# Optimization experiments

Measured on AMD Instinct MI355X. Metric: run time of the kernel, lower is better.

## Reference

```python
import jax, jax.numpy as jnp
import numpy as np

# dims: batch, seq (<=300 due to tril buffer), raw embed, model dim (hardcoded 300), experts, heads, head_size
B, T, D_IN, D, E, H, HS = 64, 300, 768, 300, 8, 4, 16
TOP_K = E // 2


def setup_inputs() -> dict:
    key = jax.random.key(0)
    ks = jax.random.split(key, 10)
    f = lambda k, s, sc: jax.random.normal(k, s, jnp.float32) * sc
    return {
        "x": jax.random.normal(ks[0], (B, T, D_IN), jnp.float32),
        "wh_bias": jnp.zeros((D_IN,), jnp.float32),
        "wh_W": f(ks[1], (D, D_IN), 0.02),              # WhitenLayer linear (no bias)
        "Wq": f(ks[2], (H, HS, D), 0.05),                # stacked per-head query weights
        "Wk": f(ks[3], (H, HS, D), 0.05),
        "Wv": f(ks[4], (H, HS, D), 0.05),
        "proj_W": f(ks[5], (D, H * HS), 0.05),
        "proj_b": jnp.zeros((D,), jnp.float32),
        "exp_W1": f(ks[6], (E, 2 * D, D), (2.0 / (2 * D)) ** 0.5),  # kaiming fan_out
        "exp_b1": jnp.zeros((E, 2 * D), jnp.float32),
        "exp_W2": f(ks[7], (E, D, 2 * D), (2.0 / D) ** 0.5),
        "exp_b2": jnp.zeros((E, D), jnp.float32),
        "w_gate": f(ks[8], (D, E), 0.02),
    }


def reference(x, wh_bias, wh_W, Wq, Wk, Wv, proj_W, proj_b,
              exp_W1, exp_b1, exp_W2, exp_b2, w_gate):
    # WhitenLayer: lin(x - bias)  (dropout identity in eval)
    xw = jnp.einsum('btd,od->bto', x - wh_bias, wh_W)          # [B,T,D]

    # MultiHeadAttention (causal, scale = C**-0.5 with C = D = 300)
    q = jnp.einsum('btd,hkd->bhtk', xw, Wq)
    k = jnp.einsum('btd,hkd->bhtk', xw, Wk)
    v = jnp.einsum('btd,hkd->bhtk', xw, Wv)
    wei = jnp.einsum('bhtk,bhsk->bhts', q, k) * (D ** -0.5)
    tril = jnp.tril(jnp.ones((T, T), bool))
    wei = jax.nn.softmax(jnp.where(tril, wei, -jnp.inf), axis=-1)
    att = jnp.einsum('bhts,bhsk->bthk', wei, v).reshape(x.shape[0], T, H * HS)
    xa = att @ proj_W.T + proj_b                               # [B,T,D]

    # noisy_top_k_gating in eval mode (no noise); masked dispatch == dense weighted sum
    logits = xa @ w_gate                                       # [B,T,E]
    topv, topi = jax.lax.top_k(logits, TOP_K)
    sel = jax.nn.one_hot(topi, E, dtype=bool).any(axis=-2)     # [B,T,E] top-k mask
    sparse = jnp.where(sel, logits, -jnp.inf)
    gprob = jax.nn.softmax(sparse, axis=-1)                    # zero on non-selected

    # all experts applied densely (forward also recomputes them all anyway)
    h = jax.nn.relu(jnp.einsum('btd,ehd->bteh', xa, exp_W1) + exp_b1)
    eo = jnp.einsum('bteh,eoh->bteo', h, exp_W2) + exp_b2      # [B,T,E,D]

    gates = jnp.einsum('bte,bteo->bto', gprob, eo)             # dispatched mixture [B,T,D]
    # forward: (gates.unsqueeze(-2) * expert_outputs).sum(-2) == gates * sum_e expert_e
    return gates * eo.sum(axis=-2)
```

## Files before the change

kernel.cpp:

```cpp
#include <hip/hip_runtime.h>
#include <cstdint>
#include <cstddef>

#define B_   64
#define T_   300
#define DIN_ 768
#define D_   300
#define E_   8
#define NTOK (B_*T_)
#define TW   6
#define SC   32

typedef __attribute__((ext_vector_type(8))) short bf8_t;
typedef __attribute__((ext_vector_type(4))) float f4_t;

__device__ __forceinline__ unsigned short f2bf(float v) {
  union { float f; unsigned u; } a; a.f = v;
  unsigned r = a.u + 0x7fff + ((a.u >> 16) & 1);
  return (unsigned short)(r >> 16);
}
__device__ __forceinline__ float bf2f(unsigned short s) {
  union { float f; unsigned u; } a; a.u = ((unsigned)s) << 16; return a.f;
}
__device__ __forceinline__ void split3(float v, unsigned short& p0,
                                       unsigned short& p1, unsigned short& p2) {
  p0 = f2bf(v);
  float r1 = v - bf2f(p0);
  p1 = f2bf(r1);
  float r2 = r1 - bf2f(p1);
  p2 = f2bf(r2);
}
__device__ __forceinline__ void split2(float v, unsigned short& p0,
                                       unsigned short& p1) {
  p0 = f2bf(v);
  p1 = f2bf(v - bf2f(p0));
}

__device__ __forceinline__ void gld16(const unsigned short* g, unsigned short* l) {
  __builtin_amdgcn_global_load_lds(
      (const __attribute__((address_space(1))) unsigned int*)g,
      (__attribute__((address_space(3))) unsigned int*)l, 16, 0, 0);
}

__global__ void biasproj_kernel(const float* __restrict__ wh_bias,
                                const float* __restrict__ wh_W,
                                float* __restrict__ bp) {
  int o = blockIdx.x * blockDim.x + threadIdx.x;
  if (o >= D_) return;
  float acc = 0.f;
  const float* row = wh_W + (size_t)o * DIN_;
  for (int d = 0; d < DIN_; ++d) acc += wh_bias[d] * row[d];
  bp[o] = -acc;
}

__global__ void split_pad(const float* __restrict__ src, unsigned short* __restrict__ dst,
                          int rows, int K, int Kp, size_t planeStride, int np) {
  int n = rows * Kp;
  for (int i = blockIdx.x * blockDim.x + threadIdx.x; i < n; i += gridDim.x * blockDim.x) {
    int r = i / Kp, c = i % Kp;
    unsigned short p0 = 0, p1 = 0, p2 = 0;
    if (c < K) split3(src[(size_t)r * K + c], p0, p1, p2);
    dst[i] = p0;
    dst[planeStride + i] = p1;
    if (np == 3) dst[2 * planeStride + i] = p2;
  }
}

template<int AFP, int EPI, int JN, int WM, int NP, int NPO, int SWZ>
__global__ __launch_bounds__(WM * 64) void mfma_gen(
    const void* __restrict__ Av, size_t aPStride, int ldA,
    const unsigned short* __restrict__ Bg, size_t bPStride,
    const float* __restrict__ bias, float* __restrict__ C,
    unsigned short* __restrict__ Po, size_t poStride, int ldPo,
    float* __restrict__ gsum, float* __restrict__ esum,
    const float* __restrict__ gate,
    int M, int N, int K) {
  constexpr int TILE_M = WM * 32;
  constexpr int BROWS  = JN * 32;
  constexpr int APB    = TILE_M * 64;
  constexpr int BPB    = BROWS * 64;
  constexpr int AINSTS = NP * APB / 1024;
  constexpr int BINSTS = NP * BPB / 1024;
  static_assert(!AFP || NP == 3, "AFP path writes 3 planes");
  __shared__ unsigned short Ap[NP][TILE_M * 32];
  __shared__ unsigned short Bp[NP][BROWS * 32];
  const int tid = threadIdx.x;
  int bxv = blockIdx.x, byv = blockIdx.y;
  if constexpr (SWZ) {
    const int nx  = gridDim.x;
    const int nwg = nx * gridDim.y;
    const int id  = byv * nx + bxv;
    const int xcd = id & 7, idx = id >> 3;
    const int q = nwg >> 3, r = nwg & 7;
    const int nid = (xcd < r) ? (xcd * (q + 1) + idx)
                              : (r * (q + 1) + (xcd - r) * q + idx);
    bxv = nid % nx;
    byv = nid / nx;
  }
  const int bm = byv * TILE_M, bn = bxv * BROWS;
  const int widx = tid >> 6;
  const int wr = (widx >> 1) * 64;
  const int wc = (widx & 1) * (JN * 16);
  const int lane = tid & 63;
  const int lr = lane & 15;
  const int kg = lane >> 4;
  const int sw = (lr >> 1) & 3;
  const int Kp = (K + 31) & ~31;
  const int arow = tid >> 1, ahalf = (tid & 1) * 16;
  const int asw = (arow >> 1) & 3;

  auto stageB = [&](int k0) {
    for (int q = widx; q < BINSTS; q += WM) {
      const int f   = q * 1024 + lane * 16;
      const int pp  = f / BPB;
      const int rem = f % BPB;
      const int row = rem >> 6;
      const int cl  = ((rem >> 4) & 3) ^ ((row >> 1) & 3);
      int brow = bn + row; if (brow >= N) brow = N - 1;
      gld16(Bg + (size_t)pp * bPStride + (size_t)brow * Kp + k0 + cl * 8,
            (unsigned short*)Bp + q * 512);
    }
  };
  auto stageA = [&](int k0) {
    if constexpr (AFP) {
      const float* Arow = (const float*)Av + (size_t)(bm + arow) * ldA + k0 + ahalf;
      #pragma unroll
      for (int u = 0; u < 4; ++u) {
        float4 qv = *(const float4*)&Arow[u * 4];
        float vv[4] = {qv.x, qv.y, qv.z, qv.w};
        unsigned short s0[4], s1[4], s2[4];
        #pragma unroll
        for (int w = 0; w < 4; ++w) split3(vv[w], s0[w], s1[w], s2[w]);
        const int k  = ahalf + u * 4;
        const int so = arow * 32 + (((k >> 3) ^ asw) << 3) + (k & 7);
        *(unsigned*)&Ap[0][so]     = (unsigned)s0[0] | ((unsigned)s0[1] << 16);
        *(unsigned*)&Ap[0][so + 2] = (unsigned)s0[2] | ((unsigned)s0[3] << 16);
        *(unsigned*)&Ap[1][so]     = (unsigned)s1[0] | ((unsigned)s1[1] << 16);
        *(unsigned*)&Ap[1][so + 2] = (unsigned)s1[2] | ((unsigned)s1[3] << 16);
        *(unsigned*)&Ap[2][so]     = (unsigned)s2[0] | ((unsigned)s2[1] << 16);
        *(unsigned*)&Ap[2][so + 2] = (unsigned)s2[2] | ((unsigned)s2[3] << 16);
      }
    } else {
      for (int q = widx; q < AINSTS; q += WM) {
        const int f   = q * 1024 + lane * 16;
        const int pp  = f / APB;
        const int rem = f % APB;
        const int row = rem >> 6;
        const int cl  = ((rem >> 4) & 3) ^ ((row >> 1) & 3);
        gld16((const unsigned short*)Av + (size_t)pp * aPStride +
                  (size_t)(bm + row) * Kp + k0 + cl * 8,
              (unsigned short*)Ap + q * 512);
      }
    }
  };

  f4_t acc[4][JN];
  #pragma unroll
  for (int i = 0; i < 4; ++i)
    #pragma unroll
    for (int j = 0; j < JN; ++j) acc[i][j] = (f4_t){0.f, 0.f, 0.f, 0.f};

  stageB(0); stageA(0);
  __syncthreads();
  for (int k0 = 0; k0 < Kp; k0 += 32) {
    bf8_t a[4][NP], b[JN][NP];
    #pragma unroll
    for (int i = 0; i < 4; ++i)
      #pragma unroll
      for (int p = 0; p < NP; ++p)
        a[i][p] = *(const bf8_t*)&Ap[p][(wr + i * 16 + lr) * 32 + ((kg ^ sw) << 3)];
    #pragma unroll
    for (int j = 0; j < JN; ++j)
      #pragma unroll
      for (int p = 0; p < NP; ++p)
        b[j][p] = *(const bf8_t*)&Bp[p][(wc + j * 16 + lr) * 32 + ((kg ^ sw) << 3)];
    __syncthreads();
    if (k0 + 32 < Kp) { stageB(k0 + 32); stageA(k0 + 32); }
    #pragma unroll
    for (int i = 0; i < 4; ++i)
      #pragma unroll
      for (int j = 0; j < JN; ++j) {
        f4_t c = acc[i][j];
        if constexpr (NP == 3) {
          c = __builtin_amdgcn_mfma_f32_16x16x32_bf16(a[i][2], b[j][0], c, 0, 0, 0);
          c = __builtin_amdgcn_mfma_f32_16x16x32_bf16(a[i][1], b[j][1], c, 0, 0, 0);
          c = __builtin_amdgcn_mfma_f32_16x16x32_bf16(a[i][0], b[j][2], c, 0, 0, 0);
          c = __builtin_amdgcn_mfma_f32_16x16x32_bf16(a[i][1], b[j][0], c, 0, 0, 0);
          c = __builtin_amdgcn_mfma_f32_16x16x32_bf16(a[i][0], b[j][1], c, 0, 0, 0);
          c = __builtin_amdgcn_mfma_f32_16x16x32_bf16(a[i][0], b[j][0], c, 0, 0, 0);
        } else {
          c = __builtin_amdgcn_mfma_f32_16x16x32_bf16(a[i][1], b[j][0], c, 0, 0, 0);
          c = __builtin_amdgcn_mfma_f32_16x16x32_bf16(a[i][0], b[j][1], c, 0, 0, 0);
          c = __builtin_amdgcn_mfma_f32_16x16x32_bf16(a[i][0], b[j][0], c, 0, 0, 0);
        }
        acc[i][j] = c;
      }
    __syncthreads();
  }
  #pragma unroll
  for (int i = 0; i < 4; ++i) {
    #pragma unroll
    for (int r = 0; r < 4; ++r) {
      const int row = bm + wr + i * 16 + kg * 4 + r;
      float g = 0.f;
      if constexpr (EPI >= 2 && EPI <= 4) g = gate[(size_t)row * E_];
      #pragma unroll
      for (int j = 0; j < JN; ++j) {
        const int col = bn + wc + j * 16 + lr;
        float v = acc[i][j][r];
        if constexpr (EPI == 0) {
          if (col < N) {
            if (bias) v += bias[col];
            C[(size_t)row * N + col] = v;
          }
        } else if constexpr (EPI == 1 || EPI == 5 || EPI == 6) {
          if (col < ldPo) {
            unsigned short p0 = 0, p1 = 0, p2 = 0;
            if (col < N) {
              v += bias[col];
              if constexpr (EPI == 1) v = fmaxf(v, 0.f);
              if constexpr (EPI == 6) C[(size_t)row * N + col] = v;
              if constexpr (NPO == 3) split3(v, p0, p1, p2);
              else                    split2(v, p0, p1);
            }
            size_t o = (size_t)row * ldPo + col;
            Po[o] = p0;
            Po[poStride + o] = p1;
            if constexpr (NPO == 3) Po[2 * poStride + o] = p2;
          }
        } else {
          if (col < N) {
            float eo = v + bias[col];
            size_t idx = (size_t)row * N + col;
            if constexpr (EPI == 2) {
              gsum[idx] = g * eo;
              esum[idx] = eo;
            } else if constexpr (EPI == 3) {
              gsum[idx] += g * eo;
              esum[idx] += eo;
            } else {
              float gs = gsum[idx] + g * eo;
              float es = esum[idx] + eo;
              C[idx] = gs * es;
            }
          }
        }
      }
    }
  }
}

__global__ __launch_bounds__(64 * TW) void attn_kernel(
    const float* __restrict__ qkv, float* __restrict__ attout) {
  const int nch_blk = T_ / TW;
  const int b   = blockIdx.x / nch_blk;
  const int tch = blockIdx.x % nch_blk;
  const int w    = threadIdx.x >> 6;
  const int lane = threadIdx.x & 63;
  const int h = lane >> 4, li = lane & 15;
  const int t    = tch * TW + w;
  const int tmax = tch * TW + TW - 1;
  __shared__ float kv[SC][68];
  __shared__ float p[TW][4][304];
  const float scale = rsqrtf((float)D_);
  const float* base = qkv + (size_t)b * T_ * 192;
  const float* qrow = base + (size_t)t * 192 + h * 16;
  const float4 q0 = *(const float4*)(qrow);
  const float4 q1 = *(const float4*)(qrow + 4);
  const float4 q2 = *(const float4*)(qrow + 8);
  const float4 q3 = *(const float4*)(qrow + 12);
  const int nch = tmax / SC + 1;

  float mmax = -1e30f;
  for (int c = 0; c < nch; ++c) {
    const int s0 = c * SC;
    __syncthreads();
    for (int i = threadIdx.x; i < SC * 16; i += 64 * TW) {
      const int r = i >> 4, c4 = (i & 15) * 4;
      int sr = s0 + r; if (sr > T_ - 1) sr = T_ - 1;
      *(float4*)&kv[r][c4] = *(const float4*)&base[(size_t)sr * 192 + 64 + c4];
    }
    __syncthreads();
    const int send = (s0 + SC - 1 < t) ? s0 + SC - 1 : t;
    for (int s = s0 + li; s <= send; s += 16) {
      const float* kr = &kv[s - s0][h * 16];
      float4 k0 = *(const float4*)(kr);
      float4 k1 = *(const float4*)(kr + 4);
      float4 k2 = *(const float4*)(kr + 8);
      float4 k3 = *(const float4*)(kr + 12);
      float acc = q0.x * k0.x + q0.y * k0.y + q0.z * k0.z + q0.w * k0.w;
      acc += q1.x * k1.x + q1.y * k1.y + q1.z * k1.z + q1.w * k1.w;
      acc += q2.x * k2.x + q2.y * k2.y + q2.z * k2.z + q2.w * k2.w;
      acc += q3.x * k3.x + q3.y * k3.y + q3.z * k3.z + q3.w * k3.w;
      acc *= scale;
      p[w][h][s] = acc;
      mmax = fmaxf(mmax, acc);
    }
  }
  #pragma unroll
  for (int m = 8; m >= 1; m >>= 1) mmax = fmaxf(mmax, __shfl_xor(mmax, m, 16));
  float lsum = 0.f;
  for (int s = li; s <= t; s += 16) {
    float e = __expf(p[w][h][s] - mmax);
    p[w][h][s] = e;
    lsum += e;
  }
  #pragma unroll
  for (int m = 8; m >= 1; m >>= 1) lsum += __shfl_xor(lsum, m, 16);
  const float inv = 1.0f / lsum;

  float o0 = 0.f, o1 = 0.f, o2 = 0.f, o3 = 0.f;
  for (int c = 0; c < nch; ++c) {
    const int s0 = c * SC;
    __syncthreads();
    for (int i = threadIdx.x; i < SC * 16; i += 64 * TW) {
      const int r = i >> 4, c4 = (i & 15) * 4;
      int sr = s0 + r; if (sr > T_ - 1) sr = T_ - 1;
      *(float4*)&kv[r][c4] = *(const float4*)&base[(size_t)sr * 192 + 128 + c4];
    }
    __syncthreads();
    const int send = (s0 + SC - 1 < t) ? s0 + SC - 1 : t;
    const int col = h * 16 + li;
    int s = s0;
    for (; s + 3 <= send; s += 4) {
      float4 pw = *(const float4*)&p[w][h][s];
      o0 += pw.x * kv[s - s0][col];
      o1 += pw.y * kv[s + 1 - s0][col];
      o2 += pw.z * kv[s + 2 - s0][col];
      o3 += pw.w * kv[s + 3 - s0][col];
    }
    for (; s <= send; ++s) o0 += p[w][h][s] * kv[s - s0][col];
  }
  attout[((size_t)b * T_ + t) * 192 + lane] = ((o0 + o1) + (o2 + o3)) * inv;
}

__global__ void logits_kernel(const float* __restrict__ xa,
                              const float* __restrict__ w_gate,
                              float* __restrict__ logits) {
  int idx = blockIdx.x * blockDim.x + threadIdx.x;
  if (idx >= NTOK * E_) return;
  int n = idx >> 3, e = idx & 7;
  const float* xr = xa + (size_t)n * D_;
  float acc = 0.f;
  for (int d = 0; d < D_; ++d) acc += xr[d] * w_gate[(size_t)d * E_ + e];
  logits[idx] = acc;
}

__global__ void gate_kernel(const float* __restrict__ logits,
                            float* __restrict__ gprob) {
  int n = blockIdx.x * blockDim.x + threadIdx.x;
  if (n >= NTOK) return;
  float l[E_];
  #pragma unroll
  for (int e = 0; e < E_; ++e) l[e] = logits[(size_t)n * E_ + e];
  bool sel[E_] = {false, false, false, false, false, false, false, false};
  for (int kk = 0; kk < E_ / 2; ++kk) {
    int bi = -1; float bv = -1e38f;
    #pragma unroll
    for (int e = 0; e < E_; ++e)
      if (!sel[e] && l[e] > bv) { bv = l[e]; bi = e; }
    sel[bi] = true;
  }
  float mx = -1e38f;
  #pragma unroll
  for (int e = 0; e < E_; ++e) if (sel[e]) mx = fmaxf(mx, l[e]);
  float s = 0.f, pp[E_];
  #pragma unroll
  for (int e = 0; e < E_; ++e) {
    pp[e] = sel[e] ? __expf(l[e] - mx) : 0.f;
    s += pp[e];
  }
  float inv = 1.0f / s;
  #pragma unroll
  for (int e = 0; e < E_; ++e) gprob[(size_t)n * E_ + e] = pp[e] * inv;
}

extern "C" void kernel_launch(void* const* d_in, const int* in_sizes, int n_in,
                              void* d_out, int out_size, void* d_ws, size_t ws_size,
                              hipStream_t stream) {
  const float* x       = (const float*)d_in[0];
  const float* wh_bias = (const float*)d_in[1];
  const float* wh_W    = (const float*)d_in[2];
  const float* Wq      = (const float*)d_in[3];
  const float* Wk      = (const float*)d_in[4];
  const float* Wv      = (const float*)d_in[5];
  const float* proj_W  = (const float*)d_in[6];
  const float* proj_b  = (const float*)d_in[7];
  const float* exp_W1  = (const float*)d_in[8];
  const float* exp_b1  = (const float*)d_in[9];
  const float* exp_W2  = (const float*)d_in[10];
  const float* exp_b2  = (const float*)d_in[11];
  const float* w_gate  = (const float*)d_in[12];
  (void)in_sizes; (void)n_in; (void)out_size;

  char* ws = (char*)d_ws;
  size_t off = 0;
  auto alloc = [&](size_t bytes) {
    void* p = ws + off; off = (off + bytes + 255) & ~(size_t)255; return p;
  };
  typedef unsigned short us;
  float* bp    = (float*)alloc(300 * 4);
  us* whp      = (us*)alloc((size_t)3 * 300 * 768 * 2);
  us* qkvp     = (us*)alloc((size_t)2 * 192 * 320 * 2);
  us* projp    = (us*)alloc((size_t)3 * 300 * 64 * 2);
  us* w1p      = (us*)alloc((size_t)2 * 4800 * 320 * 2);
  us* w2p      = (us*)alloc(((size_t)2 * 2400 * 608 + 64 * 608) * 2);
  float* gprob = (float*)alloc((size_t)NTOK * E_ * 4);
  us* xwreg    = (us*)alloc((size_t)2 * NTOK * 320 * 2);
  float* qkvb  = (float*)alloc((size_t)NTOK * 192 * 4);
  us* xap      = (us*)alloc((size_t)2 * NTOK * 320 * 2);

  float* xa = (float*)xwreg;

  const size_t xp3Bytes  = (size_t)3 * NTOK * DIN_ * 2;
  const size_t hplBytes  = (size_t)2 * NTOK * 608 * 2;
  const size_t esumBytes = (size_t)NTOK * 300 * 4;
  const size_t hplAl = (hplBytes + 255) & ~(size_t)255;
  int CHe;
  us* hpl;
  float* esum;
  us* xp3 = nullptr;
  bool preX = false;
  if (off + xp3Bytes <= ws_size) {
    char* region = ws + off;
    off += (xp3Bytes + 255) & ~(size_t)255;
    xp3  = (us*)region;
    hpl  = (us*)region;
    esum = (float*)(region + hplAl);
    CHe  = NTOK;
    preX = true;
  } else if (off + hplBytes + esumBytes <= ws_size) {
    hpl  = (us*)alloc(hplBytes);
    esum = (float*)alloc(esumBytes);
    CHe  = NTOK;
  } else {
    hpl  = xwreg;
    esum = qkvb;
    CHe  = 9600;
  }

  biasproj_kernel<<<2, 256, 0, stream>>>(wh_bias, wh_W, bp);
  auto SP = [&](const float* s, us* dbase, int rows, int K, int Kp, size_t pstr, int np) {
    int n = rows * Kp;
    int g = (n + 255) / 256; if (g > 4096) g = 4096;
    split_pad<<<g, 256, 0, stream>>>(s, dbase, rows, K, Kp, pstr, np);
  };
  SP(wh_W,   whp,              300,  768, 768, (size_t)300 * 768, 3);
  SP(Wq,     qkvp,             64,   300, 320, (size_t)192 * 320, 2);
  SP(Wk,     qkvp + 64 * 320,  64,   300, 320, (size_t)192 * 320, 2);
  SP(Wv,     qkvp + 128 * 320, 64,   300, 320, (size_t)192 * 320, 2);
  SP(proj_W, projp,            300,  64,  64,  (size_t)300 * 64, 3);
  SP(exp_W1, w1p,              4800, 300, 320, (size_t)4800 * 320, 2);
  SP(exp_W2, w2p,              2400, 600, 608, (size_t)2400 * 608, 2);

  if (preX) {
    SP(x, xp3, NTOK, DIN_, DIN_, (size_t)NTOK * DIN_, 3);
    dim3 g(5, NTOK / 128);
    mfma_gen<0, 5, 2, 4, 3, 2, 1><<<g, 256, 0, stream>>>(
        xp3, (size_t)NTOK * DIN_, 0, whp, (size_t)300 * 768, bp, nullptr,
        xwreg, (size_t)NTOK * 320, 320, nullptr, nullptr, nullptr,
        NTOK, D_, DIN_);
  } else {
    dim3 g(5, NTOK / 128);
    mfma_gen<1, 5, 2, 4, 3, 2, 1><<<g, 256, 0, stream>>>(
        x, 0, DIN_, whp, (size_t)300 * 768, bp, nullptr,
        xwreg, (size_t)NTOK * 320, 320, nullptr, nullptr, nullptr,
        NTOK, D_, DIN_);
  }
  {
    dim3 g(3, NTOK / 128);
    mfma_gen<0, 0, 2, 4, 2, 2, 1><<<g, 256, 0, stream>>>(
        xwreg, (size_t)NTOK * 320, 0, qkvp, (size_t)192 * 320, nullptr, qkvb,
        nullptr, 0, 0, nullptr, nullptr, nullptr,
        NTOK, 192, D_);
  }
  attn_kernel<<<B_ * (T_ / TW), 64 * TW, 0, stream>>>(qkvb, qkvb);

  {
    dim3 g(5, NTOK / 128);
    mfma_gen<1, 6, 2, 4, 3, 2, 1><<<g, 256, 0, stream>>>(
        qkvb, 0, 192, projp, (size_t)300 * 64, proj_b, xa,
        xap, (size_t)NTOK * 320, 320, nullptr, nullptr, nullptr,
        NTOK, D_, 64);
  }
  logits_kernel<<<(NTOK * E_ + 255) / 256, 256, 0, stream>>>(xa, w_gate, gprob);
  gate_kernel<<<(NTOK + 255) / 256, 256, 0, stream>>>(gprob, gprob);

  for (int c = 0; c < NTOK / CHe; ++c) {
    const int tok0 = c * CHe;
    float* gsum = (float*)d_out + (size_t)tok0 * D_;
    dim3 g1(5, CHe / 128);
    dim3 g2(5, CHe / 128);
    for (int e = 0; e < E_; ++e) {
      const us* w1e = w1p + (size_t)e * 600 * 320;
      const us* w2e = w2p + (size_t)e * 300 * 608;
      const float* bb1 = exp_b1 + (size_t)e * 600;
      const float* bb2 = exp_b2 + (size_t)e * D_;
      const float* gate = gprob + (size_t)tok0 * E_ + e;
      mfma_gen<0, 1, 4, 4, 2, 2, 1><<<g1, 256, 0, stream>>>(
          xap + (size_t)tok0 * 320, (size_t)NTOK * 320, 0,
          w1e, (size_t)4800 * 320, bb1, nullptr,
          hpl, (size_t)CHe * 608, 608, nullptr, nullptr, nullptr,
          CHe, 600, D_);
      if (e == 0)
        mfma_gen<0, 2, 2, 4, 2, 2, 1><<<g2, 256, 0, stream>>>(
            hpl, (size_t)CHe * 608, 0, w2e, (size_t)2400 * 608, bb2, nullptr,
            nullptr, 0, 0, gsum, esum, gate, CHe, D_, 600);
      else if (e < E_ - 1)
        mfma_gen<0, 3, 2, 4, 2, 2, 1><<<g2, 256, 0, stream>>>(
            hpl, (size_t)CHe * 608, 0, w2e, (size_t)2400 * 608, bb2, nullptr,
            nullptr, 0, 0, gsum, esum, gate, CHe, D_, 600);
      else
        mfma_gen<0, 4, 2, 4, 2, 2, 1><<<g2, 256, 0, stream>>>(
            hpl, (size_t)CHe * 608, 0, w2e, (size_t)2400 * 608, bb2,
            (float*)d_out + (size_t)tok0 * D_,
            nullptr, 0, 0, gsum, esum, gate, CHe, D_, 600);
    }
  }
}
```

Measured before the change: 964.3 us.

## Use 2-plane bf16 split for whitening GEMM, drop x pre-split, fuse gating

The whitening GEMM now splits inputs into two bf16 planes instead of three, which cuts the MFMA passes and weight storage for that stage. It also always converts x on the fly inside the GEMM instead of pre-splitting it into a large workspace buffer, which removes one full pass over x. Separately, the logits and top-k gate kernels are merged into a single per-token kernel, which drops a launch and an intermediate buffer. The 2-plane split lowers the precision of the largest input GEMM, and the fused gate kernel gives each thread more serial work.

New measurement: 901.4 us. 1.07x faster.

```diff
diff --git a/kernel.cpp b/kernel.cpp
--- a/kernel.cpp
+++ b/kernel.cpp
@@ -81,7 +81,6 @@
   constexpr int BPB    = BROWS * 64;
   constexpr int AINSTS = NP * APB / 1024;
   constexpr int BINSTS = NP * BPB / 1024;
-  static_assert(!AFP || NP == 3, "AFP path writes 3 planes");
   __shared__ unsigned short Ap[NP][TILE_M * 32];
   __shared__ unsigned short Bp[NP][BROWS * 32];
   const int tid = threadIdx.x;
@@ -130,15 +129,20 @@
         float vv[4] = {qv.x, qv.y, qv.z, qv.w};
         unsigned short s0[4], s1[4], s2[4];
         #pragma unroll
-        for (int w = 0; w < 4; ++w) split3(vv[w], s0[w], s1[w], s2[w]);
+        for (int w = 0; w < 4; ++w) {
+          if constexpr (NP == 3) split3(vv[w], s0[w], s1[w], s2[w]);
+          else                   split2(vv[w], s0[w], s1[w]);
+        }
         const int k  = ahalf + u * 4;
         const int so = arow * 32 + (((k >> 3) ^ asw) << 3) + (k & 7);
         *(unsigned*)&Ap[0][so]     = (unsigned)s0[0] | ((unsigned)s0[1] << 16);
         *(unsigned*)&Ap[0][so + 2] = (unsigned)s0[2] | ((unsigned)s0[3] << 16);
         *(unsigned*)&Ap[1][so]     = (unsigned)s1[0] | ((unsigned)s1[1] << 16);
         *(unsigned*)&Ap[1][so + 2] = (unsigned)s1[2] | ((unsigned)s1[3] << 16);
-        *(unsigned*)&Ap[2][so]     = (unsigned)s2[0] | ((unsigned)s2[1] << 16);
-        *(unsigned*)&Ap[2][so + 2] = (unsigned)s2[2] | ((unsigned)s2[3] << 16);
+        if constexpr (NP == 3) {
+          *(unsigned*)&Ap[2][so]     = (unsigned)s2[0] | ((unsigned)s2[1] << 16);
+          *(unsigned*)&Ap[2][so + 2] = (unsigned)s2[2] | ((unsigned)s2[3] << 16);
+        }
       }
     } else {
       for (int q = widx; q < AINSTS; q += WM) {
@@ -334,25 +338,19 @@
   attout[((size_t)b * T_ + t) * 192 + lane] = ((o0 + o1) + (o2 + o3)) * inv;
 }
 
-__global__ void logits_kernel(const float* __restrict__ xa,
-                              const float* __restrict__ w_gate,
-                              float* __restrict__ logits) {
-  int idx = blockIdx.x * blockDim.x + threadIdx.x;
-  if (idx >= NTOK * E_) return;
-  int n = idx >> 3, e = idx & 7;
-  const float* xr = xa + (size_t)n * D_;
-  float acc = 0.f;
-  for (int d = 0; d < D_; ++d) acc += xr[d] * w_gate[(size_t)d * E_ + e];
-  logits[idx] = acc;
-}
-
-__global__ void gate_kernel(const float* __restrict__ logits,
-                            float* __restrict__ gprob) {
+__global__ void gate_fused(const float* __restrict__ xa,
+                           const float* __restrict__ w_gate,
+                           float* __restrict__ gprob) {
   int n = blockIdx.x * blockDim.x + threadIdx.x;
   if (n >= NTOK) return;
-  float l[E_];
-  #pragma unroll
-  for (int e = 0; e < E_; ++e) l[e] = logits[(size_t)n * E_ + e];
+  const float* xr = xa + (size_t)n * D_;
+  float l[E_] = {0.f, 0.f, 0.f, 0.f, 0.f, 0.f, 0.f, 0.f};
+  for (int d = 0; d < D_; ++d) {
+    const float xv = xr[d];
+    const float* wg = w_gate + (size_t)d * E_;
+    #pragma unroll
+    for (int e = 0; e < E_; ++e) l[e] += xv * wg[e];
+  }
   bool sel[E_] = {false, false, false, false, false, false, false, false};
   for (int kk = 0; kk < E_ / 2; ++kk) {
     int bi = -1; float bv = -1e38f;
@@ -400,7 +398,7 @@
   };
   typedef unsigned short us;
   float* bp    = (float*)alloc(300 * 4);
-  us* whp      = (us*)alloc((size_t)3 * 300 * 768 * 2);
+  us* whp      = (us*)alloc((size_t)2 * 300 * 768 * 2);
   us* qkvp     = (us*)alloc((size_t)2 * 192 * 320 * 2);
   us* projp    = (us*)alloc((size_t)3 * 300 * 64 * 2);
   us* w1p      = (us*)alloc((size_t)2 * 4800 * 320 * 2);
@@ -412,24 +410,12 @@
 
   float* xa = (float*)xwreg;
 
-  const size_t xp3Bytes  = (size_t)3 * NTOK * DIN_ * 2;
   const size_t hplBytes  = (size_t)2 * NTOK * 608 * 2;
   const size_t esumBytes = (size_t)NTOK * 300 * 4;
-  const size_t hplAl = (hplBytes + 255) & ~(size_t)255;
   int CHe;
   us* hpl;
   float* esum;
-  us* xp3 = nullptr;
-  bool preX = false;
-  if (off + xp3Bytes <= ws_size) {
-    char* region = ws + off;
-    off += (xp3Bytes + 255) & ~(size_t)255;
-    xp3  = (us*)region;
-    hpl  = (us*)region;
-    esum = (float*)(region + hplAl);
-    CHe  = NTOK;
-    preX = true;
-  } else if (off + hplBytes + esumBytes <= ws_size) {
+  if (off + hplBytes + esumBytes <= ws_size) {
     hpl  = (us*)alloc(hplBytes);
     esum = (float*)alloc(esumBytes);
     CHe  = NTOK;
@@ -445,7 +431,7 @@
     int g = (n + 255) / 256; if (g > 4096) g = 4096;
     split_pad<<<g, 256, 0, stream>>>(s, dbase, rows, K, Kp, pstr, np);
   };
-  SP(wh_W,   whp,              300,  768, 768, (size_t)300 * 768, 3);
+  SP(wh_W,   whp,              300,  768, 768, (size_t)300 * 768, 2);
   SP(Wq,     qkvp,             64,   300, 320, (size_t)192 * 320, 2);
   SP(Wk,     qkvp + 64 * 320,  64,   300, 320, (size_t)192 * 320, 2);
   SP(Wv,     qkvp + 128 * 320, 64,   300, 320, (size_t)192 * 320, 2);
@@ -453,16 +439,9 @@
   SP(exp_W1, w1p,              4800, 300, 320, (size_t)4800 * 320, 2);
   SP(exp_W2, w2p,              2400, 600, 608, (size_t)2400 * 608, 2);
 
-  if (preX) {
-    SP(x, xp3, NTOK, DIN_, DIN_, (size_t)NTOK * DIN_, 3);
+  {
     dim3 g(5, NTOK / 128);
-    mfma_gen<0, 5, 2, 4, 3, 2, 1><<<g, 256, 0, stream>>>(
-        xp3, (size_t)NTOK * DIN_, 0, whp, (size_t)300 * 768, bp, nullptr,
-        xwreg, (size_t)NTOK * 320, 320, nullptr, nullptr, nullptr,
-        NTOK, D_, DIN_);
-  } else {
-    dim3 g(5, NTOK / 128);
-    mfma_gen<1, 5, 2, 4, 3, 2, 1><<<g, 256, 0, stream>>>(
+    mfma_gen<1, 5, 2, 4, 2, 2, 1><<<g, 256, 0, stream>>>(
         x, 0, DIN_, whp, (size_t)300 * 768, bp, nullptr,
         xwreg, (size_t)NTOK * 320, 320, nullptr, nullptr, nullptr,
         NTOK, D_, DIN_);
@@ -483,8 +462,7 @@
         xap, (size_t)NTOK * 320, 320, nullptr, nullptr, nullptr,
         NTOK, D_, 64);
   }
-  logits_kernel<<<(NTOK * E_ + 255) / 256, 256, 0, stream>>>(xa, w_gate, gprob);
-  gate_kernel<<<(NTOK + 255) / 256, 256, 0, stream>>>(gprob, gprob);
+  gate_fused<<<(NTOK + 255) / 256, 256, 0, stream>>>(xa, w_gate, gprob);
 
   for (int c = 0; c < NTOK / CHe; ++c) {
     const int tok0 = c * CHe;
```
